# Optimization experiments

Measured on AMD Instinct MI355X. Metric: run time of the kernel, lower is better.

The kernel has to match this reference:

```python
import jax, jax.numpy as jnp
import numpy as np

N_NODES = 50000
N_EDGES = 800000
IN_DIM, HID_DIM, OUT_DIM = 128, 256, 64


def setup_inputs() -> dict:
    key = jax.random.key(0)
    k1, k2, k3, k4 = jax.random.split(key, 4)
    x = jax.random.normal(k1, (N_NODES, IN_DIM), dtype=jnp.float32)
    edge_index = jax.random.randint(k2, (2, N_EDGES), 0, N_NODES, dtype=jnp.int32)
    # Glorot-ish scaled weights
    W1 = jax.random.normal(k3, (IN_DIM, HID_DIM), dtype=jnp.float32) * (1.0 / np.sqrt(IN_DIM))
    W2 = jax.random.normal(k4, (HID_DIM, OUT_DIM), dtype=jnp.float32) * (1.0 / np.sqrt(HID_DIM))
    b1 = jnp.zeros((HID_DIM,), dtype=jnp.float32)
    b2 = jnp.zeros((OUT_DIM,), dtype=jnp.float32)
    return {"x": x, "edge_index": edge_index, "W1": W1, "b1": b1, "W2": W2, "b2": b2}


def _gcn_conv(x, src, dst, deg_inv_sqrt, W, b):
    # transform first (PyG GCNConv order), then edge-normalized scatter-add
    h = x @ W                                        # [N, D_out]
    norm = deg_inv_sqrt[src] * deg_inv_sqrt[dst]     # [E]
    msgs = h[src] * norm[:, None]                    # [E, D_out]
    agg = jax.ops.segment_sum(msgs, dst, num_segments=x.shape[0])
    return agg + b


def reference(x, edge_index, W1, b1, W2, b2):
    n = x.shape[0]
    loops = jnp.arange(n, dtype=edge_index.dtype)
    src = jnp.concatenate([edge_index[0], loops])    # add self-loops
    dst = jnp.concatenate([edge_index[1], loops])
    deg = jax.ops.segment_sum(jnp.ones_like(dst, dtype=x.dtype), dst, num_segments=n)
    deg_inv_sqrt = jnp.where(deg > 0, jax.lax.rsqrt(jnp.maximum(deg, 1e-12)), 0.0)
    h = jax.nn.relu(_gcn_conv(x, src, dst, deg_inv_sqrt, W1, b1))
    h = _gcn_conv(h, src, dst, deg_inv_sqrt, W2, b2)
    return jax.nn.log_softmax(h, axis=1)
```

## Files before the change

### kernel.cpp

```cpp
#include <hip/hip_runtime.h>
#include <hip/hip_bf16.h>
#include <math.h>

#define N_NODES 50000
#define N_EDGES 800000
#define IN_DIM 128
#define HID_DIM 256
#define OUT_DIM 64
#define NPART 196
#define CHUNK 2048
#define NPB ((N_EDGES + CHUNK - 1) / CHUNK)
#define PREPB (N_NODES * IN_DIM / 4 / 256)

typedef __attribute__((ext_vector_type(8))) short bf16x8;
typedef __attribute__((ext_vector_type(4))) short short4v;
typedef __attribute__((ext_vector_type(4))) float f32x4;

__device__ inline short f2bf(float f) {
    unsigned u = __float_as_uint(f);
    unsigned r = (u + 0x7fffu + ((u >> 16) & 1u)) >> 16;
    return (short)r;
}
__device__ inline float bf_lo(unsigned u) { return __uint_as_float(u << 16); }
__device__ inline float bf_hi(unsigned u) { return __uint_as_float(u & 0xffff0000u); }

__global__ void hist_kernel(const int* __restrict__ dst, int* __restrict__ cnt, int E) {
    int e = blockIdx.x * blockDim.x + threadIdx.x;
    if (e < E) atomicAdd(&cnt[dst[e]], 1);
}

__global__ __launch_bounds__(256) void scan_pack_kernel(const int* __restrict__ cnt,
                                                        int* __restrict__ offs,
                                                        float* __restrict__ dis,
                                                        int* __restrict__ gcnt,
                                                        int* __restrict__ coarseBase,
                                                        int* __restrict__ coarseCnt,
                                                        int* __restrict__ coarseCursor,
                                                        const float* __restrict__ W1,
                                                        const float* __restrict__ W2,
                                                        short* __restrict__ Bp1,
                                                        short* __restrict__ Bp2, int n) {
    if (blockIdx.x >= NPART) {
        int idx = (blockIdx.x - NPART) * 256 + threadIdx.x;
        const float* W; short* Bp; int N;
        const int T1 = (IN_DIM / 32) * (HID_DIM / 16) * 64;
        const int T2 = (HID_DIM / 32) * (OUT_DIM / 16) * 64;
        if (idx < T1) { W = W1; Bp = Bp1; N = HID_DIM; }
        else { idx -= T1; if (idx >= T2) return; W = W2; Bp = Bp2; N = OUT_DIM; }
        int lane = idx & 63;
        int frag = idx >> 6;
        int ntiles = N >> 4;
        int nt = frag % ntiles;
        int kt = frag / ntiles;
        int col = nt * 16 + (lane & 15);
        int krow = kt * 32 + (lane >> 4) * 8;
        bf16x8 pk;
        #pragma unroll
        for (int j = 0; j < 8; j++) pk[j] = f2bf(W[(size_t)(krow + j) * N + col]);
        *((bf16x8*)(Bp + (size_t)idx * 8)) = pk;
        return;
    }
    __shared__ int ws[4];
    __shared__ int base;
    int tid = threadIdx.x, lane = tid & 63, wid = tid >> 6;
    int i = blockIdx.x * 256 + tid;
    int v = (i < n) ? cnt[i] : 0;
    int s = v;
    #pragma unroll
    for (int off = 1; off < 64; off <<= 1) {
        int t = __shfl_up(s, off, 64);
        if (lane >= off) s += t;
    }
    if (lane == 63) ws[wid] = s;
    __syncthreads();
    int wp = 0;
    #pragma unroll
    for (int w = 0; w < 4; w++) wp += (w < wid) ? ws[w] : 0;
    int excl = s - v + wp;
    if (tid == 255) {
        int total = excl + v;
        int b = atomicAdd(gcnt, total);
        base = b;
        coarseBase[blockIdx.x] = b;
        coarseCnt[blockIdx.x] = total;
        coarseCursor[blockIdx.x] = b;
    }
    __syncthreads();
    if (i < n) {
        offs[i] = base + excl;
        dis[i] = rsqrtf((float)v + 1.0f);
    }
}

__global__ __launch_bounds__(256) void part1_prep_kernel(const int* __restrict__ src,
                                                         const int* __restrict__ dst,
                                                         int* __restrict__ coarseCursor,
                                                         uint2* __restrict__ sedge,
                                                         const float* __restrict__ x,
                                                         const float* __restrict__ dis,
                                                         short* __restrict__ xb, int E) {
    __shared__ int cnt_l[NPART];
    __shared__ int pref[NPART];
    __shared__ int gbase[NPART];
    __shared__ int ws4[4];
    __shared__ uint2 stage[CHUNK];
    int tid = threadIdx.x;
    if (blockIdx.x >= NPB) {
        int idx = (blockIdx.x - NPB) * 256 + tid;
        int node = idx >> 5;
        float dn = dis[node];
        float4 v = ((const float4*)x)[idx];
        short4v o = {f2bf(v.x * dn), f2bf(v.y * dn), f2bf(v.z * dn), f2bf(v.w * dn)};
        ((short4v*)xb)[idx] = o;
        return;
    }
    int e0 = blockIdx.x * CHUNK;
    if (tid < NPART) cnt_l[tid] = 0;
    __syncthreads();
    int es[CHUNK / 256], ed[CHUNK / 256];
    #pragma unroll
    for (int j = 0; j < CHUNK / 256; j++) {
        int e = e0 + j * 256 + tid;
        if (e < E) {
            es[j] = src[e]; ed[j] = dst[e];
            atomicAdd(&cnt_l[ed[j] >> 8], 1);
        } else ed[j] = -1;
    }
    __syncthreads();
    int lane = tid & 63, wid = tid >> 6;
    int v = (tid < NPART) ? cnt_l[tid] : 0;
    int s = v;
    #pragma unroll
    for (int off = 1; off < 64; off <<= 1) {
        int t = __shfl_up(s, off, 64);
        if (lane >= off) s += t;
    }
    if (lane == 63) ws4[wid] = s;
    __syncthreads();
    int wp = 0;
    #pragma unroll
    for (int w = 0; w < 4; w++) wp += (w < wid) ? ws4[w] : 0;
    int excl = s - v + wp;
    if (tid < NPART) pref[tid] = excl;
    __syncthreads();
    if (tid < NPART) cnt_l[tid] = excl;
    __syncthreads();
    #pragma unroll
    for (int j = 0; j < CHUNK / 256; j++) {
        if (ed[j] >= 0) {
            int c = ed[j] >> 8;
            int p = atomicAdd(&cnt_l[c], 1);
            stage[p] = make_uint2((unsigned)es[j], (unsigned)ed[j]);
        }
    }
    __syncthreads();
    if (tid < NPART) {
        int cl = cnt_l[tid] - pref[tid];
        gbase[tid] = (cl > 0) ? atomicAdd(&coarseCursor[tid], cl) : 0;
    }
    __syncthreads();
    int total = (e0 + CHUNK <= E) ? CHUNK : (E - e0);
    for (int i = tid; i < total; i += 256) {
        uint2 ev = stage[i];
        int c = (int)(ev.y >> 8);
        sedge[gbase[c] + (i - pref[c])] = ev;
    }
}

__global__ __launch_bounds__(256) void part2_kernel(const uint2* __restrict__ sedge,
                                                    const int* __restrict__ coarseBase,
                                                    const int* __restrict__ coarseCnt,
                                                    const int* __restrict__ offs,
                                                    int* __restrict__ ssrc, int n) {
    __shared__ int cur[256];
    int b = blockIdx.x;
    int node0 = b * 256;
    int tid = threadIdx.x;
    if (node0 + tid < n) cur[tid] = offs[node0 + tid];
    __syncthreads();
    int base = coarseBase[b], cb = coarseCnt[b];
    for (int i = tid; i < cb; i += 256) {
        uint2 ev = sedge[base + i];
        int pos = atomicAdd(&cur[ev.y & 255], 1);
        ssrc[pos] = (int)ev.x;
    }
}

__global__ void agg1_kernel(const short* __restrict__ xb, const int* __restrict__ ssrc,
                            const int* __restrict__ offs, const int* __restrict__ cnt,
                            const float* __restrict__ dis, short* __restrict__ aggx, int n) {
    int lane = threadIdx.x & 63;
    int node = blockIdx.x * (blockDim.x >> 6) + (threadIdx.x >> 6);
    if (node >= n) return;
    int grp = lane >> 4, l16 = lane & 15;
    int start = offs[node], c = cnt[node];
    float acc[8] = {};
    int j = grp;
    for (; j + 4 < c; j += 8) {
        int s0 = ssrc[start + j];
        int s1 = ssrc[start + j + 4];
        uint4 p0 = *((const uint4*)(xb + (size_t)s0 * IN_DIM + l16 * 8));
        uint4 p1 = *((const uint4*)(xb + (size_t)s1 * IN_DIM + l16 * 8));
        acc[0] += bf_lo(p0.x); acc[1] += bf_hi(p0.x);
        acc[2] += bf_lo(p0.y); acc[3] += bf_hi(p0.y);
        acc[4] += bf_lo(p0.z); acc[5] += bf_hi(p0.z);
        acc[6] += bf_lo(p0.w); acc[7] += bf_hi(p0.w);
        acc[0] += bf_lo(p1.x); acc[1] += bf_hi(p1.x);
        acc[2] += bf_lo(p1.y); acc[3] += bf_hi(p1.y);
        acc[4] += bf_lo(p1.z); acc[5] += bf_hi(p1.z);
        acc[6] += bf_lo(p1.w); acc[7] += bf_hi(p1.w);
    }
    if (j < c) {
        int s0 = ssrc[start + j];
        uint4 p0 = *((const uint4*)(xb + (size_t)s0 * IN_DIM + l16 * 8));
        acc[0] += bf_lo(p0.x); acc[1] += bf_hi(p0.x);
        acc[2] += bf_lo(p0.y); acc[3] += bf_hi(p0.y);
        acc[4] += bf_lo(p0.z); acc[5] += bf_hi(p0.z);
        acc[6] += bf_lo(p0.w); acc[7] += bf_hi(p0.w);
    }
    #pragma unroll
    for (int k = 0; k < 8; k++) {
        acc[k] += __shfl_xor(acc[k], 16, 64);
        acc[k] += __shfl_xor(acc[k], 32, 64);
    }
    if (grp == 0) {
        float dn = dis[node];
        uint4 pk = *((const uint4*)(xb + (size_t)node * IN_DIM + l16 * 8));
        acc[0] += bf_lo(pk.x); acc[1] += bf_hi(pk.x);
        acc[2] += bf_lo(pk.y); acc[3] += bf_hi(pk.y);
        acc[4] += bf_lo(pk.z); acc[5] += bf_hi(pk.z);
        acc[6] += bf_lo(pk.w); acc[7] += bf_hi(pk.w);
        bf16x8 o;
        #pragma unroll
        for (int k = 0; k < 8; k++) o[k] = f2bf(acc[k] * dn);
        *((bf16x8*)(aggx + (size_t)node * IN_DIM + l16 * 8)) = o;
    }
}

template <int K, int NT, bool OUT_BF16, bool RELU, bool SCALE>
__global__ __launch_bounds__(256) void gemm_mfma(const short* __restrict__ A,
                                                 const short* __restrict__ Bp,
                                                 const float* __restrict__ bias,
                                                 const float* __restrict__ scale,
                                                 void* __restrict__ C, int M, int N) {
    int lane = threadIdx.x & 63;
    int w = threadIdx.x >> 6;
    int rowBase = blockIdx.x * 64 + w * 16;
    int arow = rowBase + (lane & 15);
    int kseg = lane >> 4;
    f32x4 acc[NT] = {};
    constexpr int KT = K / 32;
    #pragma unroll
    for (int kt = 0; kt < KT; kt++) {
        bf16x8 a = {};
        if (arow < M)
            a = *((const bf16x8*)(A + (size_t)arow * K + kt * 32 + kseg * 8));
        #pragma unroll
        for (int nt = 0; nt < NT; nt++) {
            bf16x8 b = *((const bf16x8*)(Bp + ((size_t)(kt * NT + nt) * 64 + lane) * 8));
            acc[nt] = __builtin_amdgcn_mfma_f32_16x16x32_bf16(a, b, acc[nt], 0, 0, 0);
        }
    }
    int col0 = lane & 15;
    float sc[4];
    #pragma unroll
    for (int i = 0; i < 4; i++) {
        int r = rowBase + kseg * 4 + i;
        sc[i] = (SCALE && r < M) ? scale[r] : 1.0f;
    }
    #pragma unroll
    for (int nt = 0; nt < NT; nt++) {
        int col = nt * 16 + col0;
        float bv = RELU ? bias[col] : 0.0f;
        #pragma unroll
        for (int i = 0; i < 4; i++) {
            int r = rowBase + kseg * 4 + i;
            if (r >= M) continue;
            float v = acc[nt][i];
            if (RELU) { v += bv; v = fmaxf(v, 0.0f); }
            if (SCALE) v *= sc[i];
            if (OUT_BF16) ((short*)C)[(size_t)r * N + col] = f2bf(v);
            else ((float*)C)[(size_t)r * N + col] = v;
        }
    }
}

__global__ void agg2_kernel(const float* __restrict__ h2, const int* __restrict__ ssrc,
                            const int* __restrict__ offs, const int* __restrict__ cnt,
                            const float* __restrict__ dis, const float* __restrict__ b2,
                            float* __restrict__ out, int n) {
    int lane = threadIdx.x & 63;
    int node = blockIdx.x * (blockDim.x >> 6) + (threadIdx.x >> 6);
    if (node >= n) return;
    int grp = lane >> 4, l16 = lane & 15;
    int start = offs[node], c = cnt[node];
    float acc[4] = {};
    int j = grp;
    for (; j + 4 < c; j += 8) {
        int s0 = ssrc[start + j];
        int s1 = ssrc[start + j + 4];
        float4 v0 = ((const float4*)(h2 + (size_t)s0 * OUT_DIM))[l16];
        float4 v1 = ((const float4*)(h2 + (size_t)s1 * OUT_DIM))[l16];
        acc[0] += v0.x; acc[1] += v0.y; acc[2] += v0.z; acc[3] += v0.w;
        acc[0] += v1.x; acc[1] += v1.y; acc[2] += v1.z; acc[3] += v1.w;
    }
    if (j < c) {
        int s0 = ssrc[start + j];
        float4 v0 = ((const float4*)(h2 + (size_t)s0 * OUT_DIM))[l16];
        acc[0] += v0.x; acc[1] += v0.y; acc[2] += v0.z; acc[3] += v0.w;
    }
    #pragma unroll
    for (int k = 0; k < 4; k++) {
        acc[k] += __shfl_xor(acc[k], 16, 64);
        acc[k] += __shfl_xor(acc[k], 32, 64);
    }
    float dn = dis[node];
    float4 v = ((const float4*)(h2 + (size_t)node * OUT_DIM))[l16];
    float4 bb = ((const float4*)b2)[l16];
    acc[0] = (acc[0] + v.x) * dn + bb.x; acc[1] = (acc[1] + v.y) * dn + bb.y;
    acc[2] = (acc[2] + v.z) * dn + bb.z; acc[3] = (acc[3] + v.w) * dn + bb.w;
    float m = fmaxf(fmaxf(acc[0], acc[1]), fmaxf(acc[2], acc[3]));
    #pragma unroll
    for (int off = 1; off < 16; off <<= 1) m = fmaxf(m, __shfl_xor(m, off, 64));
    float ex = expf(acc[0] - m) + expf(acc[1] - m) + expf(acc[2] - m) + expf(acc[3] - m);
    #pragma unroll
    for (int off = 1; off < 16; off <<= 1) ex += __shfl_xor(ex, off, 64);
    float ls = m + logf(ex);
    if (grp == 0) {
        float4 o = {acc[0] - ls, acc[1] - ls, acc[2] - ls, acc[3] - ls};
        ((float4*)(out + (size_t)node * OUT_DIM))[l16] = o;
    }
}

extern "C" void kernel_launch(void* const* d_in, const int* in_sizes, int n_in,
                              void* d_out, int out_size, void* d_ws, size_t ws_size,
                              hipStream_t stream) {
    const float* x  = (const float*)d_in[0];
    const int*   ei = (const int*)d_in[1];
    const float* W1 = (const float*)d_in[2];
    const float* b1 = (const float*)d_in[3];
    const float* W2 = (const float*)d_in[4];
    const float* b2 = (const float*)d_in[5];
    float* out = (float*)d_out;
    char* ws = (char*)d_ws;

    const int* srcp = ei;
    const int* dstp = ei + N_EDGES;

    int*   cnt    = (int*)(ws);
    int*   gcnt   = (int*)(ws + 200000);
    int*   offs   = (int*)(ws + 262144);
    float* dis    = (float*)(ws + 524288);
    int*   coarseBase   = (int*)(ws + 786432);
    int*   coarseCnt    = (int*)(ws + 787456);
    int*   coarseCursor = (int*)(ws + 788480);
    short* Bp1    = (short*)(ws + 1048576);
    short* Bp2    = (short*)(ws + 1114112);
    int*   ssrc   = (int*)(ws + 1179648);
    uint2* sedge  = (uint2*)(ws + 4456448);
    short* aggx   = (short*)(ws + 4456448);
    short* xb     = (short*)(ws + 17301504);
    short* h1     = (short*)(ws + 30146560);
    float* h2     = (float*)(ws + 55746560);

    hipMemsetAsync(cnt, 0, 200004, stream);

    hist_kernel<<<(N_EDGES + 255) / 256, 256, 0, stream>>>(dstp, cnt, N_EDGES);
    scan_pack_kernel<<<NPART + 24, 256, 0, stream>>>(cnt, offs, dis, gcnt,
                                                     coarseBase, coarseCnt, coarseCursor,
                                                     W1, W2, Bp1, Bp2, N_NODES);
    part1_prep_kernel<<<NPB + PREPB, 256, 0, stream>>>(srcp, dstp, coarseCursor, sedge,
                                                       x, dis, xb, N_EDGES);
    part2_kernel<<<NPART, 256, 0, stream>>>(sedge, coarseBase, coarseCnt, offs, ssrc, N_NODES);

    agg1_kernel<<<(N_NODES + 3) / 4, 256, 0, stream>>>(xb, ssrc, offs, cnt, dis, aggx, N_NODES);
    gemm_mfma<IN_DIM, HID_DIM / 16, true, true, false>
        <<<(N_NODES + 63) / 64, 256, 0, stream>>>(aggx, Bp1, b1, nullptr, h1, N_NODES, HID_DIM);

    gemm_mfma<HID_DIM, OUT_DIM / 16, false, false, true>
        <<<(N_NODES + 63) / 64, 256, 0, stream>>>(h1, Bp2, nullptr, dis, h2, N_NODES, OUT_DIM);
    agg2_kernel<<<(N_NODES + 3) / 4, 256, 0, stream>>>(h2, ssrc, offs, cnt, dis, b2, out, N_NODES);
}
```

Baseline: 243.7 us.

## Fuse both GEMMs through LDS, store h2 as bf16, unroll gathers by four

Merges the two MFMA GEMMs into one kernel. The ReLU'd hidden tile is staged in per-wave LDS and fed straight into the second GEMM, so h1 never makes a round trip through global memory. h2 is now stored in bf16 instead of fp32, which halves the gather traffic in agg2. Both aggregation loops are unrolled to keep four gathered rows in flight instead of two. The cost is lower precision for h2, extra LDS use per block, and more registers for the fused accumulators.

```diff
diff --git a/kernel.cpp b/kernel.cpp
--- a/kernel.cpp
+++ b/kernel.cpp
@@ -196,27 +196,29 @@
     int start = offs[node], c = cnt[node];
     float acc[8] = {};
     int j = grp;
-    for (; j + 4 < c; j += 8) {
+    for (; j + 12 < c; j += 16) {
         int s0 = ssrc[start + j];
         int s1 = ssrc[start + j + 4];
+        int s2 = ssrc[start + j + 8];
+        int s3 = ssrc[start + j + 12];
         uint4 p0 = *((const uint4*)(xb + (size_t)s0 * IN_DIM + l16 * 8));
         uint4 p1 = *((const uint4*)(xb + (size_t)s1 * IN_DIM + l16 * 8));
-        acc[0] += bf_lo(p0.x); acc[1] += bf_hi(p0.x);
-        acc[2] += bf_lo(p0.y); acc[3] += bf_hi(p0.y);
-        acc[4] += bf_lo(p0.z); acc[5] += bf_hi(p0.z);
-        acc[6] += bf_lo(p0.w); acc[7] += bf_hi(p0.w);
-        acc[0] += bf_lo(p1.x); acc[1] += bf_hi(p1.x);
-        acc[2] += bf_lo(p1.y); acc[3] += bf_hi(p1.y);
-        acc[4] += bf_lo(p1.z); acc[5] += bf_hi(p1.z);
-        acc[6] += bf_lo(p1.w); acc[7] += bf_hi(p1.w);
-    }
-    if (j < c) {
+        uint4 p2 = *((const uint4*)(xb + (size_t)s2 * IN_DIM + l16 * 8));
+        uint4 p3 = *((const uint4*)(xb + (size_t)s3 * IN_DIM + l16 * 8));
+        acc[0] += bf_lo(p0.x); acc[1] += bf_hi(p0.x); acc[2] += bf_lo(p0.y); acc[3] += bf_hi(p0.y);
+        acc[4] += bf_lo(p0.z); acc[5] += bf_hi(p0.z); acc[6] += bf_lo(p0.w); acc[7] += bf_hi(p0.w);
+        acc[0] += bf_lo(p1.x); acc[1] += bf_hi(p1.x); acc[2] += bf_lo(p1.y); acc[3] += bf_hi(p1.y);
+        acc[4] += bf_lo(p1.z); acc[5] += bf_hi(p1.z); acc[6] += bf_lo(p1.w); acc[7] += bf_hi(p1.w);
+        acc[0] += bf_lo(p2.x); acc[1] += bf_hi(p2.x); acc[2] += bf_lo(p2.y); acc[3] += bf_hi(p2.y);
+        acc[4] += bf_lo(p2.z); acc[5] += bf_hi(p2.z); acc[6] += bf_lo(p2.w); acc[7] += bf_hi(p2.w);
+        acc[0] += bf_lo(p3.x); acc[1] += bf_hi(p3.x); acc[2] += bf_lo(p3.y); acc[3] += bf_hi(p3.y);
+        acc[4] += bf_lo(p3.z); acc[5] += bf_hi(p3.z); acc[6] += bf_lo(p3.w); acc[7] += bf_hi(p3.w);
+    }
+    for (; j < c; j += 4) {
         int s0 = ssrc[start + j];
         uint4 p0 = *((const uint4*)(xb + (size_t)s0 * IN_DIM + l16 * 8));
-        acc[0] += bf_lo(p0.x); acc[1] += bf_hi(p0.x);
-        acc[2] += bf_lo(p0.y); acc[3] += bf_hi(p0.y);
-        acc[4] += bf_lo(p0.z); acc[5] += bf_hi(p0.z);
-        acc[6] += bf_lo(p0.w); acc[7] += bf_hi(p0.w);
+        acc[0] += bf_lo(p0.x); acc[1] += bf_hi(p0.x); acc[2] += bf_lo(p0.y); acc[3] += bf_hi(p0.y);
+        acc[4] += bf_lo(p0.z); acc[5] += bf_hi(p0.z); acc[6] += bf_lo(p0.w); acc[7] += bf_hi(p0.w);
     }
     #pragma unroll
     for (int k = 0; k < 8; k++) {
@@ -226,10 +228,8 @@
     if (grp == 0) {
         float dn = dis[node];
         uint4 pk = *((const uint4*)(xb + (size_t)node * IN_DIM + l16 * 8));
-        acc[0] += bf_lo(pk.x); acc[1] += bf_hi(pk.x);
-        acc[2] += bf_lo(pk.y); acc[3] += bf_hi(pk.y);
-        acc[4] += bf_lo(pk.z); acc[5] += bf_hi(pk.z);
-        acc[6] += bf_lo(pk.w); acc[7] += bf_hi(pk.w);
+        acc[0] += bf_lo(pk.x); acc[1] += bf_hi(pk.x); acc[2] += bf_lo(pk.y); acc[3] += bf_hi(pk.y);
+        acc[4] += bf_lo(pk.z); acc[5] += bf_hi(pk.z); acc[6] += bf_lo(pk.w); acc[7] += bf_hi(pk.w);
         bf16x8 o;
         #pragma unroll
         for (int k = 0; k < 8; k++) o[k] = f2bf(acc[k] * dn);
@@ -237,55 +237,66 @@
     }
 }
 
-template <int K, int NT, bool OUT_BF16, bool RELU, bool SCALE>
-__global__ __launch_bounds__(256) void gemm_mfma(const short* __restrict__ A,
-                                                 const short* __restrict__ Bp,
-                                                 const float* __restrict__ bias,
-                                                 const float* __restrict__ scale,
-                                                 void* __restrict__ C, int M, int N) {
+#define H1_STRIDE 264
+__global__ __launch_bounds__(256) void gemm_fused_kernel(const short* __restrict__ A,
+                                                         const short* __restrict__ Bp1,
+                                                         const short* __restrict__ Bp2,
+                                                         const float* __restrict__ b1,
+                                                         const float* __restrict__ dis,
+                                                         short* __restrict__ h2, int M) {
+    __shared__ short lds_h1[4][16][H1_STRIDE];
     int lane = threadIdx.x & 63;
     int w = threadIdx.x >> 6;
     int rowBase = blockIdx.x * 64 + w * 16;
     int arow = rowBase + (lane & 15);
     int kseg = lane >> 4;
-    f32x4 acc[NT] = {};
-    constexpr int KT = K / 32;
-    #pragma unroll
-    for (int kt = 0; kt < KT; kt++) {
+    int col0 = lane & 15;
+
+    constexpr int NT1 = HID_DIM / 16;
+    f32x4 acc1[NT1] = {};
+    #pragma unroll
+    for (int kt = 0; kt < IN_DIM / 32; kt++) {
         bf16x8 a = {};
         if (arow < M)
-            a = *((const bf16x8*)(A + (size_t)arow * K + kt * 32 + kseg * 8));
-        #pragma unroll
-        for (int nt = 0; nt < NT; nt++) {
-            bf16x8 b = *((const bf16x8*)(Bp + ((size_t)(kt * NT + nt) * 64 + lane) * 8));
-            acc[nt] = __builtin_amdgcn_mfma_f32_16x16x32_bf16(a, b, acc[nt], 0, 0, 0);
+            a = *((const bf16x8*)(A + (size_t)arow * IN_DIM + kt * 32 + kseg * 8));
+        #pragma unroll
+        for (int nt = 0; nt < NT1; nt++) {
+            bf16x8 b = *((const bf16x8*)(Bp1 + ((size_t)(kt * NT1 + nt) * 64 + lane) * 8));
+            acc1[nt] = __builtin_amdgcn_mfma_f32_16x16x32_bf16(a, b, acc1[nt], 0, 0, 0);
         }
     }
-    int col0 = lane & 15;
-    float sc[4];
+    #pragma unroll
+    for (int nt = 0; nt < NT1; nt++) {
+        float bv = b1[nt * 16 + col0];
+        #pragma unroll
+        for (int i = 0; i < 4; i++) {
+            float v = fmaxf(acc1[nt][i] + bv, 0.0f);
+            lds_h1[w][kseg * 4 + i][nt * 16 + col0] = f2bf(v);
+        }
+    }
+    constexpr int NT2 = OUT_DIM / 16;
+    f32x4 acc2[NT2] = {};
+    #pragma unroll
+    for (int kt = 0; kt < HID_DIM / 32; kt++) {
+        bf16x8 a = *((const bf16x8*)&lds_h1[w][lane & 15][kt * 32 + kseg * 8]);
+        #pragma unroll
+        for (int nt = 0; nt < NT2; nt++) {
+            bf16x8 b = *((const bf16x8*)(Bp2 + ((size_t)(kt * NT2 + nt) * 64 + lane) * 8));
+            acc2[nt] = __builtin_amdgcn_mfma_f32_16x16x32_bf16(a, b, acc2[nt], 0, 0, 0);
+        }
+    }
     #pragma unroll
     for (int i = 0; i < 4; i++) {
         int r = rowBase + kseg * 4 + i;
-        sc[i] = (SCALE && r < M) ? scale[r] : 1.0f;
-    }
-    #pragma unroll
-    for (int nt = 0; nt < NT; nt++) {
-        int col = nt * 16 + col0;
-        float bv = RELU ? bias[col] : 0.0f;
-        #pragma unroll
-        for (int i = 0; i < 4; i++) {
-            int r = rowBase + kseg * 4 + i;
-            if (r >= M) continue;
-            float v = acc[nt][i];
-            if (RELU) { v += bv; v = fmaxf(v, 0.0f); }
-            if (SCALE) v *= sc[i];
-            if (OUT_BF16) ((short*)C)[(size_t)r * N + col] = f2bf(v);
-            else ((float*)C)[(size_t)r * N + col] = v;
-        }
-    }
-}
-
-__global__ void agg2_kernel(const float* __restrict__ h2, const int* __restrict__ ssrc,
+        if (r >= M) continue;
+        float sc = dis[r];
+        #pragma unroll
+        for (int nt = 0; nt < NT2; nt++)
+            h2[(size_t)r * OUT_DIM + nt * 16 + col0] = f2bf(acc2[nt][i] * sc);
+    }
+}
+
+__global__ void agg2_kernel(const short* __restrict__ h2, const int* __restrict__ ssrc,
                             const int* __restrict__ offs, const int* __restrict__ cnt,
                             const float* __restrict__ dis, const float* __restrict__ b2,
                             float* __restrict__ out, int n) {
@@ -296,18 +307,24 @@
     int start = offs[node], c = cnt[node];
     float acc[4] = {};
     int j = grp;
-    for (; j + 4 < c; j += 8) {
+    for (; j + 12 < c; j += 16) {
         int s0 = ssrc[start + j];
         int s1 = ssrc[start + j + 4];
-        float4 v0 = ((const float4*)(h2 + (size_t)s0 * OUT_DIM))[l16];
-        float4 v1 = ((const float4*)(h2 + (size_t)s1 * OUT_DIM))[l16];
-        acc[0] += v0.x; acc[1] += v0.y; acc[2] += v0.z; acc[3] += v0.w;
-        acc[0] += v1.x; acc[1] += v1.y; acc[2] += v1.z; acc[3] += v1.w;
-    }
-    if (j < c) {
+        int s2 = ssrc[start + j + 8];
+        int s3 = ssrc[start + j + 12];
+        uint2 p0 = *((const uint2*)(h2 + (size_t)s0 * OUT_DIM + l16 * 4));
+        uint2 p1 = *((const uint2*)(h2 + (size_t)s1 * OUT_DIM + l16 * 4));
+        uint2 p2 = *((const uint2*)(h2 + (size_t)s2 * OUT_DIM + l16 * 4));
+        uint2 p3 = *((const uint2*)(h2 + (size_t)s3 * OUT_DIM + l16 * 4));
+        acc[0] += bf_lo(p0.x); acc[1] += bf_hi(p0.x); acc[2] += bf_lo(p0.y); acc[3] += bf_hi(p0.y);
+        acc[0] += bf_lo(p1.x); acc[1] += bf_hi(p1.x); acc[2] += bf_lo(p1.y); acc[3] += bf_hi(p1.y);
+        acc[0] += bf_lo(p2.x); acc[1] += bf_hi(p2.x); acc[2] += bf_lo(p2.y); acc[3] += bf_hi(p2.y);
+        acc[0] += bf_lo(p3.x); acc[1] += bf_hi(p3.x); acc[2] += bf_lo(p3.y); acc[3] += bf_hi(p3.y);
+    }
+    for (; j < c; j += 4) {
         int s0 = ssrc[start + j];
-        float4 v0 = ((const float4*)(h2 + (size_t)s0 * OUT_DIM))[l16];
-        acc[0] += v0.x; acc[1] += v0.y; acc[2] += v0.z; acc[3] += v0.w;
+        uint2 p0 = *((const uint2*)(h2 + (size_t)s0 * OUT_DIM + l16 * 4));
+        acc[0] += bf_lo(p0.x); acc[1] += bf_hi(p0.x); acc[2] += bf_lo(p0.y); acc[3] += bf_hi(p0.y);
     }
     #pragma unroll
     for (int k = 0; k < 4; k++) {
@@ -315,10 +332,12 @@
         acc[k] += __shfl_xor(acc[k], 32, 64);
     }
     float dn = dis[node];
-    float4 v = ((const float4*)(h2 + (size_t)node * OUT_DIM))[l16];
+    uint2 pv = *((const uint2*)(h2 + (size_t)node * OUT_DIM + l16 * 4));
     float4 bb = ((const float4*)b2)[l16];
-    acc[0] = (acc[0] + v.x) * dn + bb.x; acc[1] = (acc[1] + v.y) * dn + bb.y;
-    acc[2] = (acc[2] + v.z) * dn + bb.z; acc[3] = (acc[3] + v.w) * dn + bb.w;
+    acc[0] = (acc[0] + bf_lo(pv.x)) * dn + bb.x;
+    acc[1] = (acc[1] + bf_hi(pv.x)) * dn + bb.y;
+    acc[2] = (acc[2] + bf_lo(pv.y)) * dn + bb.z;
+    acc[3] = (acc[3] + bf_hi(pv.y)) * dn + bb.w;
     float m = fmaxf(fmaxf(acc[0], acc[1]), fmaxf(acc[2], acc[3]));
     #pragma unroll
     for (int off = 1; off < 16; off <<= 1) m = fmaxf(m, __shfl_xor(m, off, 64));
@@ -360,8 +379,7 @@
     uint2* sedge  = (uint2*)(ws + 4456448);
     short* aggx   = (short*)(ws + 4456448);
     short* xb     = (short*)(ws + 17301504);
-    short* h1     = (short*)(ws + 30146560);
-    float* h2     = (float*)(ws + 55746560);
+    short* h2     = (short*)(ws + 30146560);
 
     hipMemsetAsync(cnt, 0, 200004, stream);
 
@@ -374,10 +392,7 @@
     part2_kernel<<<NPART, 256, 0, stream>>>(sedge, coarseBase, coarseCnt, offs, ssrc, N_NODES);
 
     agg1_kernel<<<(N_NODES + 3) / 4, 256, 0, stream>>>(xb, ssrc, offs, cnt, dis, aggx, N_NODES);
-    gemm_mfma<IN_DIM, HID_DIM / 16, true, true, false>
-        <<<(N_NODES + 63) / 64, 256, 0, stream>>>(aggx, Bp1, b1, nullptr, h1, N_NODES, HID_DIM);
-
-    gemm_mfma<HID_DIM, OUT_DIM / 16, false, false, true>
-        <<<(N_NODES + 63) / 64, 256, 0, stream>>>(h1, Bp2, nullptr, dis, h2, N_NODES, OUT_DIM);
+    gemm_fused_kernel<<<(N_NODES + 63) / 64, 256, 0, stream>>>(aggx, Bp1, Bp2, b1, dis,
+                                                               h2, N_NODES);
     agg2_kernel<<<(N_NODES + 3) / 4, 256, 0, stream>>>(h2, ssrc, offs, cnt, dis, b2, out, N_NODES);
 }
```

Result: faster. 228.3 us (-6.3%).
